# Optimization experiments

Hardware: AMD Instinct MI355X
Metric: run time of the kernel (lower is better)

Reference implementation:

```python
import jax, jax.numpy as jnp
import numpy as np

DIM = 512
NUM_HEADS = 8
HEAD_DIM = DIM // NUM_HEADS
SCALE = HEAD_DIM ** -0.5
B, N, K_HOPS = 16, 1024, 5


def setup_inputs() -> dict:
    key = jax.random.key(0)
    ks = jax.random.split(key, 7)
    x = jax.random.normal(ks[0], (B, N, DIM), jnp.float32)
    Hstack = jax.random.uniform(ks[1], (K_HOPS, N, N), jnp.float32)
    hop_logits_attn = jax.random.normal(ks[2], (NUM_HEADS, K_HOPS), jnp.float32)
    rel_alpha = jax.random.normal(ks[3], (NUM_HEADS,), jnp.float32)
    Wqkv = jax.random.normal(ks[4], (3 * DIM, DIM), jnp.float32) * 0.02
    Wproj = jax.random.normal(ks[5], (DIM, DIM), jnp.float32) * 0.02
    bproj = jax.random.normal(ks[6], (DIM,), jnp.float32) * 0.02
    return {"x": x, "Hstack": Hstack, "hop_logits_attn": hop_logits_attn,
            "rel_alpha": rel_alpha, "Wqkv": Wqkv, "Wproj": Wproj, "bproj": bproj}


def reference(x, Hstack, hop_logits_attn, rel_alpha, Wqkv, Wproj, bproj):
    bs, n_tok, c_dim = x.shape
    # qkv projection: [B,N,3C] -> [3,B,H,N,hd]
    qkv = (x @ Wqkv.T).reshape(bs, n_tok, 3, NUM_HEADS, c_dim // NUM_HEADS)
    qkv = qkv.transpose(2, 0, 3, 1, 4)
    q, k, v = qkv[0], qkv[1], qkv[2]
    logits = jnp.einsum('bhnd,bhmd->bhnm', q, k) * SCALE  # [B,H,N,N]
    # hop-distance bias: per-head softmax mixture over K hop matrices
    w = jax.nn.softmax(hop_logits_attn, axis=-1)          # [H,K]
    B_head = jnp.einsum('hk,kij->hij', w, Hstack)          # [H,N,N]
    attn_bias = rel_alpha[:, None, None] * B_head          # [H,N,N]
    attn = jax.nn.softmax(logits + attn_bias[None], axis=-1)
    out = jnp.einsum('bhnm,bhmd->bhnd', attn, v)           # [B,H,N,hd]
    out = out.transpose(0, 2, 1, 3).reshape(bs, n_tok, c_dim)
    return out @ Wproj.T + bproj
```

## Files before the change

### kernel.cpp

```cpp
#include <hip/hip_runtime.h>
#include <hip/hip_bf16.h>
#include <hip/hip_fp16.h>
#include <stdint.h>

#define DIM   512
#define NH    8
#define HD    64
#define NB    16
#define NTOK  1024
#define KHOPS 5

typedef __attribute__((ext_vector_type(8))) short bf16x8;
typedef __attribute__((ext_vector_type(4))) float f32x4;

#define LOG2E 1.4426950408889634f

__device__ __forceinline__ unsigned short f32_to_bf16(float f) {
    unsigned int u = __builtin_bit_cast(unsigned int, f);
    unsigned int r = (u + 0x7FFFu + ((u >> 16) & 1u)) >> 16;
    return (unsigned short)r;
}

__device__ __forceinline__ float fast_exp2(float x) {
    return __builtin_amdgcn_exp2f(x);
}

#define AS1C(p) ((const __attribute__((address_space(1))) void*)(p))
#define AS3(p)  ((__attribute__((address_space(3))) void*)(p))

__global__ __launch_bounds__(256) void cvt_all(const float* __restrict__ x,
                                               const float* __restrict__ wq,
                                               const float* __restrict__ wp,
                                               unsigned short* __restrict__ xb,
                                               unsigned short* __restrict__ wqb,
                                               unsigned short* __restrict__ wpb) {
    int bid = blockIdx.x;
    const float* in; unsigned short* out; int i;
    if (bid < 8192)      { in = x;  out = xb;  i = bid * 256 + threadIdx.x; }
    else if (bid < 8960) { in = wq; out = wqb; i = (bid - 8192) * 256 + threadIdx.x; }
    else                 { in = wp; out = wpb; i = (bid - 8960) * 256 + threadIdx.x; }
    float4 v = reinterpret_cast<const float4*>(in)[i];
    ushort4 o;
    o.x = f32_to_bf16(v.x); o.y = f32_to_bf16(v.y);
    o.z = f32_to_bf16(v.z); o.w = f32_to_bf16(v.w);
    reinterpret_cast<ushort4*>(out)[i] = o;
}

__global__ __launch_bounds__(256) void bias_fused(const float* __restrict__ H,
                                                  const float* __restrict__ hop_logits,
                                                  const float* __restrict__ rel_alpha,
                                                  uint32_t* __restrict__ biast) {
    const int tid = threadIdx.x;
    const int jt = blockIdx.x, it = blockIdx.y;
    const int j0 = jt * 64, i0 = it * 64;
    float cf[NH][KHOPS];
#pragma unroll
    for (int h = 0; h < NH; ++h) {
        float m = -1e30f;
#pragma unroll
        for (int k = 0; k < KHOPS; ++k) m = fmaxf(m, hop_logits[h * KHOPS + k]);
        float s = 0.f;
#pragma unroll
        for (int k = 0; k < KHOPS; ++k) { cf[h][k] = fast_exp2((hop_logits[h * KHOPS + k] - m) * LOG2E); s += cf[h][k]; }
        float ra = rel_alpha[h] * LOG2E / s;
#pragma unroll
        for (int k = 0; k < KHOPS; ++k) cf[h][k] *= ra;
    }
    const int r = tid >> 2, c0 = (tid & 3) * 16;
    float hv[KHOPS][16];
#pragma unroll
    for (int k = 0; k < KHOPS; ++k) {
        const float4* src = reinterpret_cast<const float4*>(
            H + (size_t)k * 1048576 + (size_t)(i0 + r) * 1024 + j0 + c0);
#pragma unroll
        for (int q = 0; q < 4; ++q) {
            float4 v = src[q];
            hv[k][q * 4 + 0] = v.x; hv[k][q * 4 + 1] = v.y;
            hv[k][q * 4 + 2] = v.z; hv[k][q * 4 + 3] = v.w;
        }
    }
    for (int h = 0; h < NH; ++h) {
        uint32_t buf[8];
#pragma unroll
        for (int q = 0; q < 4; ++q) {
            float a0 = 0.f, a1 = 0.f, a2 = 0.f, a3 = 0.f;
#pragma unroll
            for (int k = 0; k < KHOPS; ++k) {
                a0 += cf[h][k] * hv[k][q * 4 + 0];
                a1 += cf[h][k] * hv[k][q * 4 + 1];
                a2 += cf[h][k] * hv[k][q * 4 + 2];
                a3 += cf[h][k] * hv[k][q * 4 + 3];
            }
            buf[q * 2 + 0] = __builtin_bit_cast(uint32_t, __floats2half2_rn(a0, a1));
            buf[q * 2 + 1] = __builtin_bit_cast(uint32_t, __floats2half2_rn(a2, a3));
        }
        uint32_t* dst = biast + ((size_t)h * 1024 + i0 + r) * 512 + ((j0 + c0) >> 1);
        uint4 w0; w0.x = buf[0]; w0.y = buf[1]; w0.z = buf[2]; w0.w = buf[3];
        uint4 w1; w1.x = buf[4]; w1.y = buf[5]; w1.z = buf[6]; w1.w = buf[7];
        reinterpret_cast<uint4*>(dst)[0] = w0;
        reinterpret_cast<uint4*>(dst)[1] = w1;
    }
}

__global__ __launch_bounds__(256) void gemm_qkv(const unsigned short* __restrict__ A,
                                                const unsigned short* __restrict__ Bw,
                                                unsigned short* __restrict__ qkv,
                                                unsigned short* __restrict__ vt) {
    __shared__ unsigned short As[128 * 32];
    __shared__ unsigned short Bs[128 * 32];
    const int tid  = threadIdx.x;
    const int lane = tid & 63;
    const int w    = tid >> 6;
    const int wr   = (w >> 1) * 64, wc = (w & 1) * 64;
    const int l15  = lane & 15, quad = lane >> 4;
    const int bid  = blockIdx.x;
    const int xcd  = bid & 7, slot = bid >> 3;
    const int m0   = (xcd * 16 + (slot & 15)) * 128;
    const int n0   = (slot >> 4) * 128;
    const int K = 512, Nn = 1536;

    f32x4 acc[4][4];
#pragma unroll
    for (int i = 0; i < 4; ++i)
#pragma unroll
        for (int j = 0; j < 4; ++j) { acc[i][j][0] = 0.f; acc[i][j][1] = 0.f; acc[i][j][2] = 0.f; acc[i][j][3] = 0.f; }

    for (int k0 = 0; k0 < K; k0 += 32) {
        __syncthreads();
#pragma unroll
        for (int t = 0; t < 2; ++t) {
            int c = t * 256 + w * 64 + lane;
            int r = c >> 2, kh = c & 3;
            const unsigned short* ga = A  + (size_t)(m0 + r) * K + k0 + kh * 8;
            const unsigned short* gb = Bw + (size_t)(n0 + r) * K + k0 + kh * 8;
            __builtin_amdgcn_global_load_lds(AS1C(ga), AS3(&As[(t * 256 + w * 64) * 8]), 16, 0, 0);
            __builtin_amdgcn_global_load_lds(AS1C(gb), AS3(&Bs[(t * 256 + w * 64) * 8]), 16, 0, 0);
        }
        __syncthreads();
        bf16x8 af[4], bfr[4];
#pragma unroll
        for (int rt = 0; rt < 4; ++rt)
            af[rt] = *reinterpret_cast<const bf16x8*>(&As[(wr + rt * 16 + l15) * 32 + quad * 8]);
#pragma unroll
        for (int ct = 0; ct < 4; ++ct)
            bfr[ct] = *reinterpret_cast<const bf16x8*>(&Bs[(wc + ct * 16 + l15) * 32 + quad * 8]);
#pragma unroll
        for (int rt = 0; rt < 4; ++rt)
#pragma unroll
            for (int ct = 0; ct < 4; ++ct)
                acc[rt][ct] = __builtin_amdgcn_mfma_f32_16x16x32_bf16(af[rt], bfr[ct], acc[rt][ct], 0, 0, 0);
    }

    if (n0 < 1024) {
#pragma unroll
        for (int rt = 0; rt < 4; ++rt)
#pragma unroll
            for (int ct = 0; ct < 4; ++ct)
#pragma unroll
                for (int reg = 0; reg < 4; ++reg) {
                    int row = m0 + wr + rt * 16 + quad * 4 + reg;
                    int col = n0 + wc + ct * 16 + l15;
                    qkv[(size_t)row * Nn + col] = f32_to_bf16(acc[rt][ct][reg]);
                }
    } else {
        const int b = m0 >> 10;
#pragma unroll
        for (int ct = 0; ct < 4; ++ct) {
            int c = n0 - 1024 + wc + ct * 16 + l15;
            unsigned short* vrow = vt + ((size_t)(b * 8) * 64 + c) * 1024;
#pragma unroll
            for (int rt = 0; rt < 4; ++rt) {
                int trow = (m0 & 1023) + wr + rt * 16 + quad * 4;
                ushort4 pk;
                pk.x = f32_to_bf16(acc[rt][ct][0]);
                pk.y = f32_to_bf16(acc[rt][ct][1]);
                pk.z = f32_to_bf16(acc[rt][ct][2]);
                pk.w = f32_to_bf16(acc[rt][ct][3]);
                *reinterpret_cast<ushort4*>(vrow + trow) = pk;
            }
        }
    }
}

__global__ __launch_bounds__(256) void gemm_proj(const unsigned short* __restrict__ A,
                                                 const unsigned short* __restrict__ Bw,
                                                 float* __restrict__ C,
                                                 const float* __restrict__ cbias) {
    __shared__ unsigned short As[128 * 32];
    __shared__ unsigned short Bs[128 * 32];
    const int tid  = threadIdx.x;
    const int lane = tid & 63;
    const int w    = tid >> 6;
    const int wr   = (w >> 1) * 64, wc = (w & 1) * 64;
    const int l15  = lane & 15, quad = lane >> 4;
    const int bid  = blockIdx.x;
    const int xcd  = bid & 7, slot = bid >> 3;
    const int m0   = (xcd * 16 + (slot & 15)) * 128;
    const int n0   = (slot >> 4) * 128;
    const int K = 512, Nn = 512;

    f32x4 acc[4][4];
#pragma unroll
    for (int i = 0; i < 4; ++i)
#pragma unroll
        for (int j = 0; j < 4; ++j) { acc[i][j][0] = 0.f; acc[i][j][1] = 0.f; acc[i][j][2] = 0.f; acc[i][j][3] = 0.f; }

    for (int k0 = 0; k0 < K; k0 += 32) {
        __syncthreads();
#pragma unroll
        for (int t = 0; t < 2; ++t) {
            int c = t * 256 + w * 64 + lane;
            int r = c >> 2, kh = c & 3;
            const unsigned short* ga = A  + (size_t)(m0 + r) * K + k0 + kh * 8;
            const unsigned short* gb = Bw + (size_t)(n0 + r) * K + k0 + kh * 8;
            __builtin_amdgcn_global_load_lds(AS1C(ga), AS3(&As[(t * 256 + w * 64) * 8]), 16, 0, 0);
            __builtin_amdgcn_global_load_lds(AS1C(gb), AS3(&Bs[(t * 256 + w * 64) * 8]), 16, 0, 0);
        }
        __syncthreads();
        bf16x8 af[4], bfr[4];
#pragma unroll
        for (int rt = 0; rt < 4; ++rt)
            af[rt] = *reinterpret_cast<const bf16x8*>(&As[(wr + rt * 16 + l15) * 32 + quad * 8]);
#pragma unroll
        for (int ct = 0; ct < 4; ++ct)
            bfr[ct] = *reinterpret_cast<const bf16x8*>(&Bs[(wc + ct * 16 + l15) * 32 + quad * 8]);
#pragma unroll
        for (int rt = 0; rt < 4; ++rt)
#pragma unroll
            for (int ct = 0; ct < 4; ++ct)
                acc[rt][ct] = __builtin_amdgcn_mfma_f32_16x16x32_bf16(af[rt], bfr[ct], acc[rt][ct], 0, 0, 0);
    }

#pragma unroll
    for (int ct = 0; ct < 4; ++ct) {
        int col = n0 + wc + ct * 16 + l15;
        float bv = cbias[col];
#pragma unroll
        for (int rt = 0; rt < 4; ++rt)
#pragma unroll
            for (int reg = 0; reg < 4; ++reg) {
                int row = m0 + wr + rt * 16 + quad * 4 + reg;
                C[(size_t)row * Nn + col] = acc[rt][ct][reg] + bv;
            }
    }
}

__global__ __launch_bounds__(256, 2) void flash_attn(const unsigned short* __restrict__ qkv,
                                                     const unsigned short* __restrict__ vt,
                                                     const uint32_t* __restrict__ biast,
                                                     unsigned short* __restrict__ aout) {
    __shared__ unsigned short Kb[2][64 * 64];
    __shared__ unsigned short Vb[2][64 * 64];
    __shared__ __align__(16) unsigned short Ps[4 * 64 * 64];
    const int tid  = threadIdx.x;
    const int lane = tid & 63, w = tid >> 6;
    const int l15  = lane & 15, quad = lane >> 4;
    const int h = blockIdx.x, qt = blockIdx.y, b = blockIdx.z;
    const int i0 = qt * 256 + w * 64;
    const float kscale = 0.125f * LOG2E;
    const int l7 = l15 & 7;
    const int psw = l7 << 3;

    bf16x8 qf[4][2];
#pragma unroll
    for (int rt = 0; rt < 4; ++rt)
#pragma unroll
        for (int ks = 0; ks < 2; ++ks)
            qf[rt][ks] = *reinterpret_cast<const bf16x8*>(
                qkv + (size_t)(b * 1024 + i0 + rt * 16 + l15) * 1536 + h * 64 + ks * 32 + quad * 8);

    f32x4 o[4][4];
    f32x4 lacc[4];
#pragma unroll
    for (int rt = 0; rt < 4; ++rt) {
#pragma unroll
        for (int nt = 0; nt < 4; ++nt) { o[rt][nt][0] = 0.f; o[rt][nt][1] = 0.f; o[rt][nt][2] = 0.f; o[rt][nt][3] = 0.f; }
        lacc[rt][0] = 0.f; lacc[rt][1] = 0.f; lacc[rt][2] = 0.f; lacc[rt][3] = 0.f;
    }

    bf16x8 ones;
#pragma unroll
    for (int e = 0; e < 8; ++e) ones[e] = (short)0x3F80;

    const int srow = lane >> 3;
    const int gch  = (lane & 7) ^ srow;
    const unsigned short* kgbase = qkv + (size_t)b * 1024 * 1536 + 512 + h * 64 + gch * 8;
    const unsigned short* vgbase = vt + (size_t)((b * 8 + h) * 64) * 1024 + gch * 8;
    const uint32_t* bb = biast + ((size_t)h * 1024 + i0) * 512;
    unsigned short* ps = &Ps[w * 64 * 64];

#pragma unroll
    for (int t = 0; t < 2; ++t) {
        int rl = w * 16 + t * 8 + srow;
        __builtin_amdgcn_global_load_lds(AS1C(kgbase + (size_t)rl * 1536),
                                         AS3(&Kb[0][(w * 16 + t * 8) * 64]), 16, 0, 0);
        __builtin_amdgcn_global_load_lds(AS1C(vgbase + (size_t)rl * 1024),
                                         AS3(&Vb[0][(w * 16 + t * 8) * 64]), 16, 0, 0);
    }

#pragma unroll 2
    for (int it = 0; it < 16; ++it) {
        const int cur = it & 1, nxt = cur ^ 1;
        const int j0 = it * 64;
        __syncthreads();

        if (it < 15) {
            const int j0n = j0 + 64;
#pragma unroll
            for (int t = 0; t < 2; ++t) {
                int rl = w * 16 + t * 8 + srow;
                __builtin_amdgcn_global_load_lds(AS1C(kgbase + (size_t)(j0n + rl) * 1536),
                                                 AS3(&Kb[nxt][(w * 16 + t * 8) * 64]), 16, 0, 0);
                __builtin_amdgcn_global_load_lds(AS1C(vgbase + (size_t)rl * 1024 + j0n),
                                                 AS3(&Vb[nxt][(w * 16 + t * 8) * 64]), 16, 0, 0);
            }
        }

        uint2 bl[4][4];
#pragma unroll
        for (int rt = 0; rt < 4; ++rt)
#pragma unroll
            for (int jt = 0; jt < 4; ++jt)
                bl[rt][jt] = *reinterpret_cast<const uint2*>(
                    bb + (size_t)(rt * 16 + l15) * 512 + (j0 >> 1) + jt * 8 + quad * 2);

#pragma unroll
        for (int rp = 0; rp < 2; ++rp) {
            f32x4 s[2][4];
#pragma unroll
            for (int r2 = 0; r2 < 2; ++r2)
#pragma unroll
                for (int jt = 0; jt < 4; ++jt) { s[r2][jt][0] = 0.f; s[r2][jt][1] = 0.f; s[r2][jt][2] = 0.f; s[r2][jt][3] = 0.f; }
#pragma unroll
            for (int ks = 0; ks < 2; ++ks) {
                bf16x8 kf[4];
#pragma unroll
                for (int jt = 0; jt < 4; ++jt)
                    kf[jt] = *reinterpret_cast<const bf16x8*>(
                        &Kb[cur][(jt * 16 + l15) * 64 + (((ks * 4 + quad) ^ l7) * 8)]);
#pragma unroll
                for (int r2 = 0; r2 < 2; ++r2)
#pragma unroll
                    for (int jt = 0; jt < 4; ++jt)
                        s[r2][jt] = __builtin_amdgcn_mfma_f32_16x16x32_bf16(kf[jt], qf[rp * 2 + r2][ks], s[r2][jt], 0, 0, 0);
            }
#pragma unroll
            for (int r2 = 0; r2 < 2; ++r2)
#pragma unroll
                for (int jt = 0; jt < 4; ++jt) {
                    const int rt = rp * 2 + r2;
                    float2 f0 = __half22float2(__builtin_bit_cast(__half2, bl[rt][jt].x));
                    float2 f1 = __half22float2(__builtin_bit_cast(__half2, bl[rt][jt].y));
                    float p0 = fast_exp2(__builtin_fmaf(s[r2][jt][0], kscale, f0.x));
                    float p1 = fast_exp2(__builtin_fmaf(s[r2][jt][1], kscale, f0.y));
                    float p2 = fast_exp2(__builtin_fmaf(s[r2][jt][2], kscale, f1.x));
                    float p3 = fast_exp2(__builtin_fmaf(s[r2][jt][3], kscale, f1.y));
                    uint32_t u0 = (uint32_t)f32_to_bf16(p0) | ((uint32_t)f32_to_bf16(p1) << 16);
                    uint32_t u1 = (uint32_t)f32_to_bf16(p2) | ((uint32_t)f32_to_bf16(p3) << 16);
                    uint2 pk; pk.x = u0; pk.y = u1;
                    *reinterpret_cast<uint2*>(
                        ps + (((rt * 16 + l15) * 64 + jt * 16 + quad * 4) ^ psw)) = pk;
                }
        }

#pragma unroll
        for (int ks = 0; ks < 2; ++ks) {
            bf16x8 vf[4];
#pragma unroll
            for (int nt = 0; nt < 4; ++nt)
                vf[nt] = *reinterpret_cast<const bf16x8*>(
                    &Vb[cur][(nt * 16 + l15) * 64 + (((ks * 4 + quad) ^ l7) * 8)]);
#pragma unroll
            for (int rt = 0; rt < 4; ++rt) {
                bf16x8 pf = *reinterpret_cast<const bf16x8*>(
                    ps + (((rt * 16 + l15) * 64 + ks * 32 + quad * 8) ^ psw));
#pragma unroll
                for (int nt = 0; nt < 4; ++nt)
                    o[rt][nt] = __builtin_amdgcn_mfma_f32_16x16x32_bf16(pf, vf[nt], o[rt][nt], 0, 0, 0);
                lacc[rt] = __builtin_amdgcn_mfma_f32_16x16x32_bf16(pf, ones, lacc[rt], 0, 0, 0);
            }
        }
    }

#pragma unroll
    for (int rt = 0; rt < 4; ++rt) {
        float inv[4];
#pragma unroll
        for (int reg = 0; reg < 4; ++reg) inv[reg] = 1.f / lacc[rt][reg];
#pragma unroll
        for (int nt = 0; nt < 4; ++nt)
#pragma unroll
            for (int reg = 0; reg < 4; ++reg) {
                int row = b * 1024 + i0 + rt * 16 + quad * 4 + reg;
                int col = h * 64 + nt * 16 + l15;
                aout[(size_t)row * 512 + col] = f32_to_bf16(o[rt][nt][reg] * inv[reg]);
            }
    }
}

extern "C" void kernel_launch(void* const* d_in, const int* in_sizes, int n_in,
                              void* d_out, int out_size, void* d_ws, size_t ws_size,
                              hipStream_t stream) {
    const float* x          = (const float*)d_in[0];
    const float* Hstack     = (const float*)d_in[1];
    const float* hop_logits = (const float*)d_in[2];
    const float* rel_alpha  = (const float*)d_in[3];
    const float* Wqkv       = (const float*)d_in[4];
    const float* Wproj      = (const float*)d_in[5];
    const float* bproj      = (const float*)d_in[6];
    float* out = (float*)d_out;

    char* ws = (char*)d_ws;
    unsigned short* xb    = (unsigned short*)(ws);
    unsigned short* wqb   = (unsigned short*)(ws + 16777216);
    unsigned short* wpb   = (unsigned short*)(ws + 18350080);
    unsigned short* qkvb  = (unsigned short*)(ws + 18874368);
    unsigned short* vtb   = (unsigned short*)(ws + 69206016);
    uint32_t*       biast = (uint32_t*)(ws + 85983232);
    unsigned short* aoutb = (unsigned short*)(ws + 102760448);

    cvt_all<<<9216, 256, 0, stream>>>(x, Wqkv, Wproj, xb, wqb, wpb);

    bias_fused<<<dim3(16, 16), 256, 0, stream>>>(Hstack, hop_logits, rel_alpha, biast);

    gemm_qkv<<<1536, 256, 0, stream>>>(xb, wqb, qkvb, vtb);

    flash_attn<<<dim3(8, 4, 16), 256, 0, stream>>>(qkvb, vtb, biast, aoutb);

    gemm_proj<<<512, 256, 0, stream>>>(aoutb, wpb, out, bproj);
}
```

Baseline: 266.9 us.

## Software-pipeline attention loop into two row halves with MFMA priority hints

Splits the per-tile work of the attention inner loop into two 32-row halves. The second half's QK^T MFMAs and the first half's PV MFMAs are issued while the exp/convert VALU work of the other half is pending, with s_setprio raised around the MFMA blocks. The aim is to overlap transcendental/VALU softmax work with matrix-core work. It also swaps the manual bf16 rounding for the HIP intrinsic packed conversion, which may map to a hardware cvt instruction. This adds register pressure from holding two sets of score and bias fragments at once.

```diff
diff --git a/kernel.cpp b/kernel.cpp
--- a/kernel.cpp
+++ b/kernel.cpp
@@ -19,6 +19,21 @@
     unsigned int u = __builtin_bit_cast(unsigned int, f);
     unsigned int r = (u + 0x7FFFu + ((u >> 16) & 1u)) >> 16;
     return (unsigned short)r;
+}
+
+__device__ __forceinline__ uint32_t pack_bf16x2(float lo, float hi) {
+    float2 f; f.x = lo; f.y = hi;
+    __hip_bfloat162 h = __float22bfloat162_rn(f);
+    uint32_t r;
+    __builtin_memcpy(&r, &h, 4);
+    return r;
+}
+
+__device__ __forceinline__ unsigned short cvt_bf16(float f) {
+    __hip_bfloat16 h = __float2bfloat16(f);
+    unsigned short r;
+    __builtin_memcpy(&r, &h, 2);
+    return r;
 }
 
 __device__ __forceinline__ float fast_exp2(float x) {
@@ -316,51 +331,76 @@
             }
         }
 
-        uint2 bl[4][4];
-#pragma unroll
-        for (int rt = 0; rt < 4; ++rt)
+        uint2 bl0[2][4];
+#pragma unroll
+        for (int r2 = 0; r2 < 2; ++r2)
 #pragma unroll
             for (int jt = 0; jt < 4; ++jt)
-                bl[rt][jt] = *reinterpret_cast<const uint2*>(
-                    bb + (size_t)(rt * 16 + l15) * 512 + (j0 >> 1) + jt * 8 + quad * 2);
-
-#pragma unroll
-        for (int rp = 0; rp < 2; ++rp) {
-            f32x4 s[2][4];
+                bl0[r2][jt] = *reinterpret_cast<const uint2*>(
+                    bb + (size_t)(r2 * 16 + l15) * 512 + (j0 >> 1) + jt * 8 + quad * 2);
+
+        f32x4 s0[2][4];
+#pragma unroll
+        for (int r2 = 0; r2 < 2; ++r2)
+#pragma unroll
+            for (int jt = 0; jt < 4; ++jt) { s0[r2][jt][0] = 0.f; s0[r2][jt][1] = 0.f; s0[r2][jt][2] = 0.f; s0[r2][jt][3] = 0.f; }
+        __builtin_amdgcn_s_setprio(1);
+#pragma unroll
+        for (int ks = 0; ks < 2; ++ks) {
+            bf16x8 kf[4];
+#pragma unroll
+            for (int jt = 0; jt < 4; ++jt)
+                kf[jt] = *reinterpret_cast<const bf16x8*>(
+                    &Kb[cur][(jt * 16 + l15) * 64 + (((ks * 4 + quad) ^ l7) * 8)]);
 #pragma unroll
             for (int r2 = 0; r2 < 2; ++r2)
 #pragma unroll
-                for (int jt = 0; jt < 4; ++jt) { s[r2][jt][0] = 0.f; s[r2][jt][1] = 0.f; s[r2][jt][2] = 0.f; s[r2][jt][3] = 0.f; }
-#pragma unroll
-            for (int ks = 0; ks < 2; ++ks) {
-                bf16x8 kf[4];
-#pragma unroll
                 for (int jt = 0; jt < 4; ++jt)
-                    kf[jt] = *reinterpret_cast<const bf16x8*>(
-                        &Kb[cur][(jt * 16 + l15) * 64 + (((ks * 4 + quad) ^ l7) * 8)]);
-#pragma unroll
-                for (int r2 = 0; r2 < 2; ++r2)
-#pragma unroll
-                    for (int jt = 0; jt < 4; ++jt)
-                        s[r2][jt] = __builtin_amdgcn_mfma_f32_16x16x32_bf16(kf[jt], qf[rp * 2 + r2][ks], s[r2][jt], 0, 0, 0);
-            }
+                    s0[r2][jt] = __builtin_amdgcn_mfma_f32_16x16x32_bf16(kf[jt], qf[r2][ks], s0[r2][jt], 0, 0, 0);
+        }
+        __builtin_amdgcn_s_setprio(0);
+
+#pragma unroll
+        for (int r2 = 0; r2 < 2; ++r2)
+#pragma unroll
+            for (int jt = 0; jt < 4; ++jt) {
+                float2 f0 = __half22float2(__builtin_bit_cast(__half2, bl0[r2][jt].x));
+                float2 f1 = __half22float2(__builtin_bit_cast(__half2, bl0[r2][jt].y));
+                float p0 = fast_exp2(__builtin_fmaf(s0[r2][jt][0], kscale, f0.x));
+                float p1 = fast_exp2(__builtin_fmaf(s0[r2][jt][1], kscale, f0.y));
+                float p2 = fast_exp2(__builtin_fmaf(s0[r2][jt][2], kscale, f1.x));
+                float p3 = fast_exp2(__builtin_fmaf(s0[r2][jt][3], kscale, f1.y));
+                uint2 pk; pk.x = pack_bf16x2(p0, p1); pk.y = pack_bf16x2(p2, p3);
+                *reinterpret_cast<uint2*>(
+                    ps + (((r2 * 16 + l15) * 64 + jt * 16 + quad * 4) ^ psw)) = pk;
+            }
+
+        uint2 bl1[2][4];
+#pragma unroll
+        for (int r2 = 0; r2 < 2; ++r2)
+#pragma unroll
+            for (int jt = 0; jt < 4; ++jt)
+                bl1[r2][jt] = *reinterpret_cast<const uint2*>(
+                    bb + (size_t)((2 + r2) * 16 + l15) * 512 + (j0 >> 1) + jt * 8 + quad * 2);
+
+        f32x4 s1[2][4];
+#pragma unroll
+        for (int r2 = 0; r2 < 2; ++r2)
+#pragma unroll
+            for (int jt = 0; jt < 4; ++jt) { s1[r2][jt][0] = 0.f; s1[r2][jt][1] = 0.f; s1[r2][jt][2] = 0.f; s1[r2][jt][3] = 0.f; }
+        __builtin_amdgcn_s_setprio(1);
+#pragma unroll
+        for (int ks = 0; ks < 2; ++ks) {
+            bf16x8 kf[4];
+#pragma unroll
+            for (int jt = 0; jt < 4; ++jt)
+                kf[jt] = *reinterpret_cast<const bf16x8*>(
+                    &Kb[cur][(jt * 16 + l15) * 64 + (((ks * 4 + quad) ^ l7) * 8)]);
 #pragma unroll
             for (int r2 = 0; r2 < 2; ++r2)
 #pragma unroll
-                for (int jt = 0; jt < 4; ++jt) {
-                    const int rt = rp * 2 + r2;
-                    float2 f0 = __half22float2(__builtin_bit_cast(__half2, bl[rt][jt].x));
-                    float2 f1 = __half22float2(__builtin_bit_cast(__half2, bl[rt][jt].y));
-                    float p0 = fast_exp2(__builtin_fmaf(s[r2][jt][0], kscale, f0.x));
-                    float p1 = fast_exp2(__builtin_fmaf(s[r2][jt][1], kscale, f0.y));
-                    float p2 = fast_exp2(__builtin_fmaf(s[r2][jt][2], kscale, f1.x));
-                    float p3 = fast_exp2(__builtin_fmaf(s[r2][jt][3], kscale, f1.y));
-                    uint32_t u0 = (uint32_t)f32_to_bf16(p0) | ((uint32_t)f32_to_bf16(p1) << 16);
-                    uint32_t u1 = (uint32_t)f32_to_bf16(p2) | ((uint32_t)f32_to_bf16(p3) << 16);
-                    uint2 pk; pk.x = u0; pk.y = u1;
-                    *reinterpret_cast<uint2*>(
-                        ps + (((rt * 16 + l15) * 64 + jt * 16 + quad * 4) ^ psw)) = pk;
-                }
+                for (int jt = 0; jt < 4; ++jt)
+                    s1[r2][jt] = __builtin_amdgcn_mfma_f32_16x16x32_bf16(kf[jt], qf[2 + r2][ks], s1[r2][jt], 0, 0, 0);
         }
 
 #pragma unroll
@@ -371,7 +411,7 @@
                 vf[nt] = *reinterpret_cast<const bf16x8*>(
                     &Vb[cur][(nt * 16 + l15) * 64 + (((ks * 4 + quad) ^ l7) * 8)]);
 #pragma unroll
-            for (int rt = 0; rt < 4; ++rt) {
+            for (int rt = 0; rt < 2; ++rt) {
                 bf16x8 pf = *reinterpret_cast<const bf16x8*>(
                     ps + (((rt * 16 + l15) * 64 + ks * 32 + quad * 8) ^ psw));
 #pragma unroll
@@ -380,6 +420,42 @@
                 lacc[rt] = __builtin_amdgcn_mfma_f32_16x16x32_bf16(pf, ones, lacc[rt], 0, 0, 0);
             }
         }
+        __builtin_amdgcn_s_setprio(0);
+
+#pragma unroll
+        for (int r2 = 0; r2 < 2; ++r2)
+#pragma unroll
+            for (int jt = 0; jt < 4; ++jt) {
+                float2 f0 = __half22float2(__builtin_bit_cast(__half2, bl1[r2][jt].x));
+                float2 f1 = __half22float2(__builtin_bit_cast(__half2, bl1[r2][jt].y));
+                float p0 = fast_exp2(__builtin_fmaf(s1[r2][jt][0], kscale, f0.x));
+                float p1 = fast_exp2(__builtin_fmaf(s1[r2][jt][1], kscale, f0.y));
+                float p2 = fast_exp2(__builtin_fmaf(s1[r2][jt][2], kscale, f1.x));
+                float p3 = fast_exp2(__builtin_fmaf(s1[r2][jt][3], kscale, f1.y));
+                uint2 pk; pk.x = pack_bf16x2(p0, p1); pk.y = pack_bf16x2(p2, p3);
+                *reinterpret_cast<uint2*>(
+                    ps + ((((2 + r2) * 16 + l15) * 64 + jt * 16 + quad * 4) ^ psw)) = pk;
+            }
+
+        __builtin_amdgcn_s_setprio(1);
+#pragma unroll
+        for (int ks = 0; ks < 2; ++ks) {
+            bf16x8 vf[4];
+#pragma unroll
+            for (int nt = 0; nt < 4; ++nt)
+                vf[nt] = *reinterpret_cast<const bf16x8*>(
+                    &Vb[cur][(nt * 16 + l15) * 64 + (((ks * 4 + quad) ^ l7) * 8)]);
+#pragma unroll
+            for (int rt = 2; rt < 4; ++rt) {
+                bf16x8 pf = *reinterpret_cast<const bf16x8*>(
+                    ps + (((rt * 16 + l15) * 64 + ks * 32 + quad * 8) ^ psw));
+#pragma unroll
+                for (int nt = 0; nt < 4; ++nt)
+                    o[rt][nt] = __builtin_amdgcn_mfma_f32_16x16x32_bf16(pf, vf[nt], o[rt][nt], 0, 0, 0);
+                lacc[rt] = __builtin_amdgcn_mfma_f32_16x16x32_bf16(pf, ones, lacc[rt], 0, 0, 0);
+            }
+        }
+        __builtin_amdgcn_s_setprio(0);
     }
 
 #pragma unroll
@@ -393,7 +469,7 @@
             for (int reg = 0; reg < 4; ++reg) {
                 int row = b * 1024 + i0 + rt * 16 + quad * 4 + reg;
                 int col = h * 64 + nt * 16 + l15;
-                aout[(size_t)row * 512 + col] = f32_to_bf16(o[rt][nt][reg] * inv[reg]);
+                aout[(size_t)row * 512 + col] = cvt_bf16(o[rt][nt][reg] * inv[reg]);
             }
     }
 }
```

Result: slower. 275.1 us (+3.1%).
